# Kernel optimization log

Hardware: AMD Instinct MI355X
Metric: run time of the kernel (lower is better)

Reference implementation:

```python
import jax, jax.numpy as jnp
import numpy as np

DIM = 768
NUM_HEADS = 12
DIM_HEAD = 64
INNER = NUM_HEADS * DIM_HEAD  # 768
SCALE = DIM_HEAD ** -0.5


def setup_inputs() -> dict:
    key = jax.random.key(0)
    k1, k2, k3 = jax.random.split(key, 3)
    B, N = 8, 1024
    x = jax.random.normal(k1, (B, N, DIM), dtype=jnp.float32)
    # Linear(dim, 3*inner_dim, bias=False): weight shape (out, in) torch-style
    w_qkv = jax.random.normal(k2, (3 * INNER, DIM), dtype=jnp.float32) * (DIM ** -0.5)
    # proj: Linear(inner_dim, dim, bias=False)
    w_proj = jax.random.normal(k3, (DIM, INNER), dtype=jnp.float32) * (INNER ** -0.5)
    return {"x": x, "w_qkv": w_qkv, "w_proj": w_proj}


def reference(x, w_qkv, w_proj):
    B, N, C = x.shape
    H, dh = NUM_HEADS, DIM_HEAD
    # qkv projection: (B,N,C) @ (C, 3*inner) -> (B,N,3*inner)
    qkv = jnp.einsum('bnc,oc->bno', x, w_qkv)
    qkv = qkv.reshape(B, N, 3, H, dh).transpose(2, 0, 3, 1, 4)  # (3,B,H,N,dh)
    q, k, v = qkv[0], qkv[1], qkv[2]
    # attention scores (B,H,N,N)
    attn_scores = jnp.einsum('bhnd,bhmd->bhnm', q, k) * SCALE
    attn_probs = jax.nn.softmax(attn_scores, axis=-1)
    # attention output (B,H,N,dh) -> (B,N,inner)
    attn_out = jnp.einsum('bhnm,bhmd->bhnd', attn_probs, v)
    attn_out = attn_out.transpose(0, 2, 1, 3).reshape(B, N, H * dh)
    out = jnp.einsum('bni,oi->bno', attn_out, w_proj)
    return out
```

## Files before the change

kernel.cpp:

```cpp
#include <hip/hip_runtime.h>
#include <stdint.h>

typedef unsigned short u16;
typedef __attribute__((ext_vector_type(8))) short short8;
typedef __attribute__((ext_vector_type(4))) short short4v;
typedef __attribute__((ext_vector_type(4))) float f32x4;

#define LOG2E 1.44269504088896340736f

#define Bb 8
#define NSEQ 1024
#define DIMC 768
#define NH 12
#define DH 64
#define INNER 768
#define MTOT (Bb*NSEQ)
#define QKVN (3*INNER)
#define HEADS_TOT (Bb*NH)
#define QKV_PART ((size_t)Bb*NH*NSEQ*DH)

static __device__ inline u16 f2bf(float f) {
    uint32_t u = __builtin_bit_cast(uint32_t, f);
    uint32_t r = (u + 0x7fffu + ((u >> 16) & 1u)) >> 16;
    return (u16)r;
}

static __device__ __forceinline__ uint32_t pkbf(float f0, float f1) {
    uint32_t u0 = __builtin_bit_cast(uint32_t, f0) + 0x8000u;
    uint32_t u1 = __builtin_bit_cast(uint32_t, f1) + 0x8000u;
    return __builtin_amdgcn_perm(u1, u0, 0x07060302u);
}

#if __has_builtin(__builtin_amdgcn_mfma_f32_16x16x16bf16_1k)
static __device__ __forceinline__ f32x4 mfma16(short4v a, short4v b, f32x4 c) {
    return __builtin_amdgcn_mfma_f32_16x16x16bf16_1k(a, b, c, 0, 0, 0);
}
#else
static __device__ __forceinline__ f32x4 mfma16(short4v a, short4v b, f32x4 c) {
    asm volatile("v_mfma_f32_16x16x16_bf16 %0, %1, %2, %0\n\ts_nop 7\n\ts_nop 7"
                 : "+v"(c) : "v"(a), "v"(b));
    return c;
}
#endif

typedef __attribute__((address_space(1))) const void gas_void;
typedef __attribute__((address_space(3))) void las_void;
static __device__ __forceinline__ void async16(u16* lds, const u16* g) {
    __builtin_amdgcn_global_load_lds((gas_void*)(uintptr_t)g,
                                     (las_void*)(uintptr_t)lds, 16, 0, 0);
}

static __device__ __forceinline__ void wait_vm0() {
    __builtin_amdgcn_s_waitcnt(0x0f70);
}

#define NX8  786432
#define NWQ8 221184
#define NWP8 73728
#define NCVT (NX8 + NWQ8 + NWP8)
__global__ __launch_bounds__(256) void cvt_all(const float* __restrict__ x,
                                               const float* __restrict__ wq,
                                               const float* __restrict__ wp,
                                               u16* __restrict__ xb,
                                               u16* __restrict__ wqb,
                                               u16* __restrict__ wpb) {
    int i = blockIdx.x * 256 + threadIdx.x;
    const float* s; u16* d; int j;
    if (i < NX8) { s = x; d = xb; j = i; }
    else if (i < NX8 + NWQ8) { s = wq; d = wqb; j = i - NX8; }
    else { s = wp; d = wpb; j = i - NX8 - NWQ8; }
    const float4* s4 = (const float4*)s;
    float4 a = s4[2 * j], b = s4[2 * j + 1];
    float v[8] = {a.x, a.y, a.z, a.w, b.x, b.y, b.z, b.w};
    u16 o[8];
#pragma unroll
    for (int t = 0; t < 8; t++) o[t] = f2bf(v[t]);
    ((uint4*)d)[j] = *(const uint4*)o;
}

#define BK 32
__global__ __launch_bounds__(512, 4) void gemm_qkv(const u16* __restrict__ A,
                                                   const u16* __restrict__ Bm,
                                                   u16* __restrict__ qkv) {
    __shared__ u16 As[2][128 * BK];
    __shared__ u16 Bs[2][256 * BK];
    const int tid = threadIdx.x;
    const int w = tid >> 6, lane = tid & 63, quad = lane >> 4, l16 = lane & 15;
    const int wr = w >> 2, wc = w & 3;
    const int m0 = blockIdx.y * 128;
    const int n0 = blockIdx.x * 256;
    const int K = DIMC;

    const int rl = lane >> 2, cc = lane & 3;
    const int ra = w * 16 + rl;
    const u16* agp = A + (size_t)(m0 + ra) * K + ((cc - ((ra >> 1) & 3)) & 3) * 8;
    const int aslot = (w * 16) * BK;
    const u16* bgp[2]; int bslot[2];
#pragma unroll
    for (int j = 0; j < 2; j++) {
        int rb = w * 32 + j * 16 + rl;
        bgp[j] = Bm + (size_t)(n0 + rb) * K + ((cc - ((rb >> 1) & 3)) & 3) * 8;
        bslot[j] = (w * 32 + j * 16) * BK;
    }

    const int swz = ((quad + ((l16 >> 1) & 3)) & 3) * 8;
    int aoff[4], boff[4];
#pragma unroll
    for (int t = 0; t < 4; t++) {
        aoff[t] = (wr * 64 + t * 16 + l16) * BK + swz;
        boff[t] = (wc * 64 + t * 16 + l16) * BK + swz;
    }

    async16(&As[0][aslot], agp);
    async16(&Bs[0][bslot[0]], bgp[0]);
    async16(&Bs[0][bslot[1]], bgp[1]);

    f32x4 acc[4][4] = {};
    const int NIT = K / BK;
    for (int it = 0; it < NIT; ++it) {
        const int cur = it & 1, nxt = cur ^ 1;
        wait_vm0();
        __syncthreads();
        if (it + 1 < NIT) {
            int ktn = (it + 1) * BK;
            async16(&As[nxt][aslot], agp + ktn);
            async16(&Bs[nxt][bslot[0]], bgp[0] + ktn);
            async16(&Bs[nxt][bslot[1]], bgp[1] + ktn);
        }
        short8 af[4], bf[4];
#pragma unroll
        for (int t = 0; t < 4; t++) af[t] = *(const short8*)(&As[cur][aoff[t]]);
#pragma unroll
        for (int t = 0; t < 4; t++) bf[t] = *(const short8*)(&Bs[cur][boff[t]]);
#pragma unroll
        for (int mt = 0; mt < 4; mt++)
#pragma unroll
            for (int nt = 0; nt < 4; nt++)
                acc[mt][nt] = __builtin_amdgcn_mfma_f32_16x16x32_bf16(af[mt], bf[nt],
                                                                      acc[mt][nt], 0, 0, 0);
    }

#pragma unroll
    for (int nt = 0; nt < 4; nt++) {
        int o = n0 + wc * 64 + nt * 16 + l16;
        int which = o / 768;
        int rem = o - which * 768;
        int h = rem >> 6, d = rem & 63;
        if (which == 2) {
            u16* vt = qkv + 2 * QKV_PART;
#pragma unroll
            for (int mt = 0; mt < 4; mt++) {
                int m = m0 + wr * 64 + mt * 16 + quad * 4;
                int bb = m >> 10, ns = m & 1023;
                alignas(8) u16 pk[4];
#pragma unroll
                for (int r = 0; r < 4; r++) pk[r] = f2bf(acc[mt][nt][r]);
                *(uint2*)(vt + ((size_t)(bb * NH + h) * DH + d) * NSEQ + ns) =
                    *(const uint2*)pk;
            }
        } else {
            float sc = (which == 0) ? (0.125f * LOG2E) : 1.0f;
#pragma unroll
            for (int mt = 0; mt < 4; mt++)
#pragma unroll
                for (int r = 0; r < 4; r++) {
                    int m = m0 + wr * 64 + mt * 16 + quad * 4 + r;
                    int bb = m >> 10, ns = m & 1023;
                    size_t idx = (size_t)which * QKV_PART +
                                 (((size_t)(bb * NH + h) * NSEQ + ns) << 6) + d;
                    qkv[idx] = f2bf(acc[mt][nt][r] * sc);
                }
        }
    }
}

__global__ __launch_bounds__(256) void gemm_proj(const u16* __restrict__ A,
                                                 const u16* __restrict__ Bm,
                                                 float* __restrict__ Co) {
    __shared__ u16 As[128 * BK];
    __shared__ u16 Bs[128 * BK];
    const int tid = threadIdx.x;
    const int w = tid >> 6, lane = tid & 63, quad = lane >> 4, l16 = lane & 15;
    const int wr = w >> 1, wc = w & 1;
    const int m0 = blockIdx.y * 128;
    const int n0 = blockIdx.x * 128;
    const int K = INNER, N = DIMC;

    const int rl = lane >> 2, cc = lane & 3;
    const u16* ag[2]; const u16* bg[2]; u16* al[2]; u16* bl[2];
#pragma unroll
    for (int j = 0; j < 2; j++) {
        int r = w * 32 + j * 16 + rl;
        int c = ((cc - ((r >> 1) & 3)) & 3) * 8;
        ag[j] = A + (size_t)(m0 + r) * K + c;
        bg[j] = Bm + (size_t)(n0 + r) * K + c;
        al[j] = As + (w * 32 + j * 16) * BK;
        bl[j] = Bs + (w * 32 + j * 16) * BK;
    }
    const int swz = ((quad + ((l16 >> 1) & 3)) & 3) * 8;
    int aoff[4], boff[4];
#pragma unroll
    for (int t = 0; t < 4; t++) {
        aoff[t] = (wr * 64 + t * 16 + l16) * BK + swz;
        boff[t] = (wc * 64 + t * 16 + l16) * BK + swz;
    }

    f32x4 acc[4][4] = {};
    for (int kt = 0; kt < K; kt += BK) {
        __syncthreads();
#pragma unroll
        for (int j = 0; j < 2; j++) {
            async16(al[j], ag[j] + kt);
            async16(bl[j], bg[j] + kt);
        }
        __syncthreads();
        short8 af[4], bf[4];
#pragma unroll
        for (int t = 0; t < 4; t++) af[t] = *(const short8*)(As + aoff[t]);
#pragma unroll
        for (int t = 0; t < 4; t++) bf[t] = *(const short8*)(Bs + boff[t]);
#pragma unroll
        for (int mt = 0; mt < 4; mt++)
#pragma unroll
            for (int nt = 0; nt < 4; nt++)
                acc[mt][nt] = __builtin_amdgcn_mfma_f32_16x16x32_bf16(af[mt], bf[nt],
                                                                      acc[mt][nt], 0, 0, 0);
    }
#pragma unroll
    for (int mt = 0; mt < 4; mt++)
#pragma unroll
        for (int nt = 0; nt < 4; nt++) {
            int o = n0 + wc * 64 + nt * 16 + l16;
#pragma unroll
            for (int r = 0; r < 4; r++) {
                int m = m0 + wr * 64 + mt * 16 + quad * 4 + r;
                Co[(size_t)m * N + o] = acc[mt][nt][r];
            }
        }
}

__global__ __launch_bounds__(256) void attn_kernel(const u16* __restrict__ qkv,
                                                   u16* __restrict__ attn) {
    __shared__ u16 Ks[64 * 64];
    __shared__ u16 Vs[64 * 64];

    const int tid = threadIdx.x;
    const int w = tid >> 6, lane = tid & 63, quad = lane >> 4, l16 = lane & 15;
    const int bh = blockIdx.x, qt = blockIdx.y;
    const size_t headoff = (size_t)bh * NSEQ * DH;
    const u16* Qp = qkv + headoff;
    const u16* Kp = qkv + QKV_PART + headoff;
    const u16* Vtp = qkv + 2 * QKV_PART + headoff;
    const int q0 = qt * 128 + w * 32;

    const int rl8 = lane >> 3, cc8 = lane & 7;
    const u16* kg[2]; const u16* vg[2]; u16* kl[2]; u16* vl[2];
#pragma unroll
    for (int j = 0; j < 2; j++) {
        int r = w * 16 + j * 8 + rl8;
        int c = ((cc8 - r) & 7) * 8;
        kg[j] = Kp + (size_t)r * DH + c;
        vg[j] = Vtp + (size_t)r * NSEQ + c;
        kl[j] = Ks + (w * 16 + j * 8) * 64;
        vl[j] = Vs + (w * 16 + j * 8) * 64;
    }

    const int sw0 = ((quad + l16) & 7) * 8;
    const int sw1 = ((quad + 4 + l16) & 7) * 8;

    short8 qf[2][2];
#pragma unroll
    for (int mf = 0; mf < 2; mf++) {
        qf[mf][0] = *(const short8*)(Qp + (size_t)(q0 + mf * 16 + l16) * DH + quad * 8);
        qf[mf][1] = *(const short8*)(Qp + (size_t)(q0 + mf * 16 + l16) * DH + 32 + quad * 8);
    }

    f32x4 oacc[2][4] = {};
    float lsum[2] = {0.f, 0.f};

    for (int kt = 0; kt < NSEQ; kt += 64) {
        __syncthreads();
#pragma unroll
        for (int j = 0; j < 2; j++) {
            async16(kl[j], kg[j] + (size_t)kt * DH);
            async16(vl[j], vg[j] + kt);
        }
        __syncthreads();

        short8 kf[4][2];
#pragma unroll
        for (int nt = 0; nt < 4; nt++) {
            const u16* kr = Ks + (nt * 16 + l16) * 64;
            kf[nt][0] = *(const short8*)(kr + sw0);
            kf[nt][1] = *(const short8*)(kr + sw1);
        }
        short4v vf[4][4];
#pragma unroll
        for (int nt2 = 0; nt2 < 4; nt2++) {
            int row = nt2 * 16 + l16;
#pragma unroll
            for (int c = 0; c < 4; c++) {
                int off = row * 64 + (((c * 2 + (quad >> 1) + row) & 7) << 3) + (quad & 1) * 4;
                vf[nt2][c] = *(const short4v*)(Vs + off);
            }
        }

#pragma unroll
        for (int mf = 0; mf < 2; mf++) {
            f32x4 st[4];
#pragma unroll
            for (int nt = 0; nt < 4; nt++) {
                f32x4 z = {};
                z = __builtin_amdgcn_mfma_f32_16x16x32_bf16(kf[nt][0], qf[mf][0], z, 0, 0, 0);
                z = __builtin_amdgcn_mfma_f32_16x16x32_bf16(kf[nt][1], qf[mf][1], z, 0, 0, 0);
                st[nt] = z;
            }
            short4v pf[4];
#pragma unroll
            for (int c = 0; c < 4; c++) {
                float p0 = __builtin_amdgcn_exp2f(st[c][0]);
                float p1 = __builtin_amdgcn_exp2f(st[c][1]);
                float p2 = __builtin_amdgcn_exp2f(st[c][2]);
                float p3 = __builtin_amdgcn_exp2f(st[c][3]);
                lsum[mf] += (p0 + p1) + (p2 + p3);
                uint2 u = {pkbf(p0, p1), pkbf(p2, p3)};
                pf[c] = __builtin_bit_cast(short4v, u);
            }
#pragma unroll
            for (int nt2 = 0; nt2 < 4; nt2++)
#pragma unroll
                for (int c = 0; c < 4; c++)
                    oacc[mf][nt2] = mfma16(vf[nt2][c], pf[c], oacc[mf][nt2]);
        }
    }

#pragma unroll
    for (int mf = 0; mf < 2; mf++) {
        float v = lsum[mf];
        v += __shfl_xor(v, 16);
        v += __shfl_xor(v, 32);
        lsum[mf] = 1.0f / v;
    }

    const int b = bh / NH, h = bh - (bh / NH) * NH;
#pragma unroll
    for (int mf = 0; mf < 2; mf++) {
        int q = q0 + mf * 16 + l16;
        float inv = lsum[mf];
#pragma unroll
        for (int nt2 = 0; nt2 < 4; nt2++) {
            uint2 u = {pkbf(oacc[mf][nt2][0] * inv, oacc[mf][nt2][1] * inv),
                       pkbf(oacc[mf][nt2][2] * inv, oacc[mf][nt2][3] * inv)};
            int d = nt2 * 16 + quad * 4;
            *(uint2*)(attn + ((size_t)(b * NSEQ + q)) * INNER + h * DH + d) = u;
        }
    }
}

extern "C" void kernel_launch(void* const* d_in, const int* in_sizes, int n_in,
                              void* d_out, int out_size, void* d_ws, size_t ws_size,
                              hipStream_t stream) {
    const float* x = (const float*)d_in[0];
    const float* w_qkv = (const float*)d_in[1];
    const float* w_proj = (const float*)d_in[2];
    float* out = (float*)d_out;

    u16* xb = (u16*)d_ws;
    u16* wqkvb = xb + 6291456;
    u16* wprojb = wqkvb + 1769472;
    u16* qkvb = wprojb + 589824;
    u16* attnb = qkvb + 18874368;

    cvt_all<<<NCVT / 256, 256, 0, stream>>>(x, w_qkv, w_proj, xb, wqkvb, wprojb);

    dim3 g1(QKVN / 256, MTOT / 128);
    gemm_qkv<<<g1, 512, 0, stream>>>(xb, wqkvb, qkvb);

    dim3 g2(HEADS_TOT, NSEQ / 128);
    attn_kernel<<<g2, 256, 0, stream>>>(qkvb, attnb);

    dim3 g3(INNER / 128, MTOT / 128);
    gemm_proj<<<g3, 256, 0, stream>>>(attnb, wprojb, out);
}
```

Measured before the change: 198.5 us.

## Double-buffer LDS tiles in proj GEMM and attention; remap QKV GEMM blocks per XCD

Converts the projection GEMM and attention K/V loops to double-buffered shared memory, so the async global-to-LDS loads for the next tile are issued before computing on the current one. This hides global load latency behind MFMA work and saves one barrier per iteration. It also remaps QKV GEMM block indices so consecutive M tiles land on the same XCD for better L2 reuse of A rows. In exchange, LDS use per block doubles, which may lower occupancy.

```diff
diff --git a/kernel.cpp b/kernel.cpp
--- a/kernel.cpp
+++ b/kernel.cpp
@@ -87,8 +87,10 @@
     const int tid = threadIdx.x;
     const int w = tid >> 6, lane = tid & 63, quad = lane >> 4, l16 = lane & 15;
     const int wr = w >> 2, wc = w & 3;
-    const int m0 = blockIdx.y * 128;
-    const int n0 = blockIdx.x * 256;
+    const int bid = blockIdx.x + 9 * blockIdx.y;
+    const int xcd = bid & 7, j9 = bid >> 3;
+    const int m0 = (8 * xcd + j9 / 9) * 128;
+    const int n0 = (j9 % 9) * 256;
     const int K = DIMC;
 
     const int rl = lane >> 2, cc = lane & 3;
@@ -177,8 +179,8 @@
 __global__ __launch_bounds__(256) void gemm_proj(const u16* __restrict__ A,
                                                  const u16* __restrict__ Bm,
                                                  float* __restrict__ Co) {
-    __shared__ u16 As[128 * BK];
-    __shared__ u16 Bs[128 * BK];
+    __shared__ u16 As[2][128 * BK];
+    __shared__ u16 Bs[2][128 * BK];
     const int tid = threadIdx.x;
     const int w = tid >> 6, lane = tid & 63, quad = lane >> 4, l16 = lane & 15;
     const int wr = w >> 1, wc = w & 1;
@@ -187,15 +189,14 @@
     const int K = INNER, N = DIMC;
 
     const int rl = lane >> 2, cc = lane & 3;
-    const u16* ag[2]; const u16* bg[2]; u16* al[2]; u16* bl[2];
+    const u16* ag[2]; const u16* bg[2]; int sl[2];
 #pragma unroll
     for (int j = 0; j < 2; j++) {
         int r = w * 32 + j * 16 + rl;
         int c = ((cc - ((r >> 1) & 3)) & 3) * 8;
         ag[j] = A + (size_t)(m0 + r) * K + c;
         bg[j] = Bm + (size_t)(n0 + r) * K + c;
-        al[j] = As + (w * 32 + j * 16) * BK;
-        bl[j] = Bs + (w * 32 + j * 16) * BK;
+        sl[j] = (w * 32 + j * 16) * BK;
     }
     const int swz = ((quad + ((l16 >> 1) & 3)) & 3) * 8;
     int aoff[4], boff[4];
@@ -205,20 +206,31 @@
         boff[t] = (wc * 64 + t * 16 + l16) * BK + swz;
     }
 
+#pragma unroll
+    for (int j = 0; j < 2; j++) {
+        async16(&As[0][sl[j]], ag[j]);
+        async16(&Bs[0][sl[j]], bg[j]);
+    }
+
     f32x4 acc[4][4] = {};
-    for (int kt = 0; kt < K; kt += BK) {
+    const int NIT = K / BK;
+    for (int it = 0; it < NIT; ++it) {
+        const int cur = it & 1, nxt = cur ^ 1;
+        wait_vm0();
         __syncthreads();
-#pragma unroll
-        for (int j = 0; j < 2; j++) {
-            async16(al[j], ag[j] + kt);
-            async16(bl[j], bg[j] + kt);
-        }
-        __syncthreads();
+        if (it + 1 < NIT) {
+            int ktn = (it + 1) * BK;
+#pragma unroll
+            for (int j = 0; j < 2; j++) {
+                async16(&As[nxt][sl[j]], ag[j] + ktn);
+                async16(&Bs[nxt][sl[j]], bg[j] + ktn);
+            }
+        }
         short8 af[4], bf[4];
 #pragma unroll
-        for (int t = 0; t < 4; t++) af[t] = *(const short8*)(As + aoff[t]);
-#pragma unroll
-        for (int t = 0; t < 4; t++) bf[t] = *(const short8*)(Bs + boff[t]);
+        for (int t = 0; t < 4; t++) af[t] = *(const short8*)(&As[cur][aoff[t]]);
+#pragma unroll
+        for (int t = 0; t < 4; t++) bf[t] = *(const short8*)(&Bs[cur][boff[t]]);
 #pragma unroll
         for (int mt = 0; mt < 4; mt++)
 #pragma unroll
@@ -241,8 +253,8 @@
 
 __global__ __launch_bounds__(256) void attn_kernel(const u16* __restrict__ qkv,
                                                    u16* __restrict__ attn) {
-    __shared__ u16 Ks[64 * 64];
-    __shared__ u16 Vs[64 * 64];
+    __shared__ u16 Ks[2][64 * 64];
+    __shared__ u16 Vs[2][64 * 64];
 
     const int tid = threadIdx.x;
     const int w = tid >> 6, lane = tid & 63, quad = lane >> 4, l16 = lane & 15;
@@ -254,15 +266,14 @@
     const int q0 = qt * 128 + w * 32;
 
     const int rl8 = lane >> 3, cc8 = lane & 7;
-    const u16* kg[2]; const u16* vg[2]; u16* kl[2]; u16* vl[2];
+    const u16* kg[2]; const u16* vg[2]; int ksl[2];
 #pragma unroll
     for (int j = 0; j < 2; j++) {
         int r = w * 16 + j * 8 + rl8;
         int c = ((cc8 - r) & 7) * 8;
         kg[j] = Kp + (size_t)r * DH + c;
         vg[j] = Vtp + (size_t)r * NSEQ + c;
-        kl[j] = Ks + (w * 16 + j * 8) * 64;
-        vl[j] = Vs + (w * 16 + j * 8) * 64;
+        ksl[j] = (w * 16 + j * 8) * 64;
     }
 
     const int sw0 = ((quad + l16) & 7) * 8;
@@ -275,22 +286,33 @@
         qf[mf][1] = *(const short8*)(Qp + (size_t)(q0 + mf * 16 + l16) * DH + 32 + quad * 8);
     }
 
+#pragma unroll
+    for (int j = 0; j < 2; j++) {
+        async16(&Ks[0][ksl[j]], kg[j]);
+        async16(&Vs[0][ksl[j]], vg[j]);
+    }
+
     f32x4 oacc[2][4] = {};
     float lsum[2] = {0.f, 0.f};
 
-    for (int kt = 0; kt < NSEQ; kt += 64) {
+    const int NIT = NSEQ / 64;
+    for (int it = 0; it < NIT; ++it) {
+        const int cur = it & 1, nxt = cur ^ 1;
+        wait_vm0();
         __syncthreads();
-#pragma unroll
-        for (int j = 0; j < 2; j++) {
-            async16(kl[j], kg[j] + (size_t)kt * DH);
-            async16(vl[j], vg[j] + kt);
-        }
-        __syncthreads();
+        if (it + 1 < NIT) {
+            int ktn = (it + 1) * 64;
+#pragma unroll
+            for (int j = 0; j < 2; j++) {
+                async16(&Ks[nxt][ksl[j]], kg[j] + (size_t)ktn * DH);
+                async16(&Vs[nxt][ksl[j]], vg[j] + ktn);
+            }
+        }
 
         short8 kf[4][2];
 #pragma unroll
         for (int nt = 0; nt < 4; nt++) {
-            const u16* kr = Ks + (nt * 16 + l16) * 64;
+            const u16* kr = &Ks[cur][(nt * 16 + l16) * 64];
             kf[nt][0] = *(const short8*)(kr + sw0);
             kf[nt][1] = *(const short8*)(kr + sw1);
         }
@@ -301,7 +323,7 @@
 #pragma unroll
             for (int c = 0; c < 4; c++) {
                 int off = row * 64 + (((c * 2 + (quad >> 1) + row) & 7) << 3) + (quad & 1) * 4;
-                vf[nt2][c] = *(const short4v*)(Vs + off);
+                vf[nt2][c] = *(const short4v*)(&Vs[cur][off]);
             }
         }
 
```

New measurement: 187.3 us. -5.7%, faster.
